# Kernel tuning notes

Measured on AMD Instinct MI355X. Metric: run time of the kernel, lower is better.

Reference implementation:

```python
import jax, jax.numpy as jnp
import numpy as np

K = 20  # top-K neighbors per stock
SLOPE = 0.2  # LeakyReLU negative slope


def _gru_layer(x, Wih, Whh, bih, bhh):
    # x: [N, T, D]; PyTorch GRU gate order: r, z, n
    H = Whh.shape[1]
    def step(h, xt):
        gi = xt @ Wih.T + bih            # [N, 3H]
        gh = h @ Whh.T + bhh             # [N, 3H]
        ir, iz, inn = jnp.split(gi, 3, axis=1)
        hr, hz, hn = jnp.split(gh, 3, axis=1)
        r = jax.nn.sigmoid(ir + hr)
        z = jax.nn.sigmoid(iz + hz)
        n = jnp.tanh(inn + r * hn)
        h_new = (1.0 - z) * n + z * h
        return h_new, h_new
    h0 = jnp.zeros((x.shape[0], H), x.dtype)
    _, ys = jax.lax.scan(step, h0, jnp.swapaxes(x, 0, 1))
    return jnp.swapaxes(ys, 0, 1)        # [N, T, H]


def _cos_sim(x, y):
    # torch: xy / (||x|| ||y||^T), NaN (0/0) replaced by 0
    xy = x @ y.T
    xn = jnp.sqrt(jnp.sum(x * x, axis=1, keepdims=True))
    yn = jnp.sqrt(jnp.sum(y * y, axis=1, keepdims=True))
    denom = xn @ yn.T
    safe = jnp.where(denom == 0.0, 1.0, denom)
    return jnp.where(denom == 0.0, 0.0, xy / safe)


def setup_inputs() -> dict:
    key = jax.random.key(0)
    ks = jax.random.split(key, 20)
    N, T, F, H = 4096, 64, 32, 128
    def rn(k, shape, scale=0.1):
        return jax.random.normal(k, shape, dtype=jnp.float32) * scale
    b01 = lambda n: jnp.full((n,), 0.1, jnp.float32)
    return {
        'x': jax.random.normal(ks[0], (N, T, F), dtype=jnp.float32),
        'Wih0': rn(ks[1], (3 * H, F)), 'Whh0': rn(ks[2], (3 * H, H)),
        'bih0': rn(ks[3], (3 * H,)), 'bhh0': rn(ks[4], (3 * H,)),
        'Wih1': rn(ks[5], (3 * H, H)), 'Whh1': rn(ks[6], (3 * H, H)),
        'bih1': rn(ks[7], (3 * H,)), 'bhh1': rn(ks[8], (3 * H,)),
        'W_hc': rn(ks[9], (H, H)), 'b_hc': b01(H),
        'W_hs': rn(ks[10], (H, H)), 'b_hs': b01(H),
        'W_fore': rn(ks[11], (H, H)), 'b_fore': b01(H),
        'W_back': rn(ks[12], (H, H)), 'b_back': b01(H),
        'W_indi': rn(ks[13], (H, H)), 'b_indi': b01(H),
        'W_out': rn(ks[14], (1, H)), 'b_out': b01(1),
    }


def reference(x, Wih0, Whh0, bih0, bhh0, Wih1, Whh1, bih1, bhh1,
              W_hc, b_hc, W_hs, b_hs, W_fore, b_fore, W_back, b_back,
              W_indi, b_indi, W_out, b_out):
    lrelu = lambda v: jax.nn.leaky_relu(v, SLOPE)
    h = _gru_layer(x, Wih0, Whh0, bih0, bhh0)
    h = _gru_layer(h, Wih1, Whh1, bih1, bhh1)
    g = h[:, -1, :]                                   # [N, H] last-step GRU output
    N = g.shape[0]

    sim = _cos_sim(g, g)                              # [N, N]
    diag = jnp.diagonal(sim)
    sim_off = sim * (1.0 - jnp.eye(N, dtype=sim.dtype))

    # top-K (by |sim|) neighbor mask via scatter
    cols = jax.lax.top_k(jnp.abs(sim_off), K)[1]      # [N, K]
    rows = jnp.repeat(jnp.arange(N), K)
    mask = jnp.zeros((N, N), sim.dtype).at[rows, cols.reshape(-1)].set(1.0)

    tks = sim_off * mask
    col_nz = (jnp.sum(tks, axis=0) != 0).astype(sim.dtype)
    tks = tks + jnp.diag(col_nz * diag)

    # concept features; zero rows (empty concepts) are masked instead of filtered
    concept_raw = tks.T @ g                           # [N, H]
    valid = (jnp.sum(concept_raw, axis=1) != 0).astype(g.dtype)
    cf = lrelu(concept_raw @ W_hc.T + b_hc) * valid[:, None]

    attn = jax.nn.softmax(_cos_sim(g, cf), axis=0)    # softmax over stocks per concept
    hs = lrelu((attn @ cf) @ W_hs.T + b_hs)
    back = lrelu(hs @ W_back.T + b_back)
    fore = lrelu(hs @ W_fore.T + b_fore)
    indi = lrelu((g - back) @ W_indi.T + b_indi)
    pred = (fore + indi) @ W_out.T + b_out            # [N, 1]
    return pred.squeeze(-1)
```

## Files before the change

### kernel.cpp

```cpp
#include <hip/hip_runtime.h>


typedef float f32x4 __attribute__((ext_vector_type(4)));
typedef short s16x8 __attribute__((ext_vector_type(8)));
typedef unsigned short u16;
typedef unsigned long long u64;

#define DEVFN static __device__ __forceinline__

DEVFN u16 f2bf(float f) {
  union { float f; unsigned u; } v; v.f = f;
  return (u16)((v.u + 0x7FFFu + ((v.u >> 16) & 1u)) >> 16);
}

DEVFN f32x4 mfma16(s16x8 a, s16x8 b, f32x4 c) {
  return __builtin_amdgcn_mfma_f32_16x16x32_bf16(a, b, c, 0, 0, 0);
}

DEVFN float sigmf(float x) { return __builtin_amdgcn_rcpf(1.f + __expf(-x)); }
DEVFN float tanhf_fast(float x) {
  float e = __expf(2.f * x);
  return 1.f - 2.f * __builtin_amdgcn_rcpf(e + 1.f);
}
DEVFN float lrelu(float v) { return v > 0.f ? v : 0.2f * v; }

__global__ void cvt_all(const float* __restrict__ w0, const float* __restrict__ w1,
                        const float* __restrict__ w2, const float* __restrict__ w3,
                        const float* __restrict__ w4, const float* __restrict__ w5,
                        const float* __restrict__ w6, const float* __restrict__ w7,
                        u16* __restrict__ dst) {
  int i = blockIdx.x * 256 + threadIdx.x;
  if (i >= 225280) return;
  float v;
  if      (i < 12288)  v = w0[i];
  else if (i < 61440)  v = w1[i - 12288];
  else if (i < 110592) v = w2[i - 61440];
  else if (i < 159744) v = w3[i - 110592];
  else if (i < 176128) v = w4[i - 159744];
  else if (i < 192512) v = w5[i - 176128];
  else if (i < 208896) v = w6[i - 192512];
  else                 v = w7[i - 208896];
  dst[i] = f2bf(v);
}

__launch_bounds__(512, 2)
__global__ void gru_fused(const float* __restrict__ x,
                          const u16* __restrict__ Wih0, const u16* __restrict__ Whh0,
                          const float* __restrict__ bih0, const float* __restrict__ bhh0,
                          const u16* __restrict__ Wih1, const u16* __restrict__ Whh1,
                          const float* __restrict__ bih1, const float* __restrict__ bhh1,
                          float* __restrict__ g_out)
{
  const int tid  = threadIdx.x;
  const int w    = tid >> 6;
  const int l    = tid & 63;
  const int quad = l >> 4;
  const int l16  = l & 15;
  const int r0   = blockIdx.x * 16;
  const int c    = w * 16 + l16;

  __shared__ u16 sh_x[16 * 40];
  __shared__ u16 sh_h0[2][16 * 136];
  __shared__ u16 sh_h1[2][16 * 136];

  s16x8 B0ih[3];
  s16x8 B0hh[3][4];
  s16x8 B1ih[3][4];
  s16x8 B1hh[3][4];
  float bi0[3], bh0[3], bi1[3], bh1[3];
#pragma unroll
  for (int g = 0; g < 3; ++g) {
    int j = g * 128 + c;
    bi0[g] = bih0[j]; bh0[g] = bhh0[j];
    bi1[g] = bih1[j]; bh1[g] = bhh1[j];
    B0ih[g] = *(const s16x8*)(Wih0 + j * 32 + quad * 8);
#pragma unroll
    for (int kk = 0; kk < 4; ++kk) {
      B0hh[g][kk] = *(const s16x8*)(Whh0 + j * 128 + kk * 32 + quad * 8);
      B1ih[g][kk] = *(const s16x8*)(Wih1 + j * 128 + kk * 32 + quad * 8);
      B1hh[g][kk] = *(const s16x8*)(Whh1 + j * 128 + kk * 32 + quad * 8);
    }
  }
  float h0reg[4] = {0.f, 0.f, 0.f, 0.f};
  float h1reg[4] = {0.f, 0.f, 0.f, 0.f};
  for (int idx = tid; idx < 16 * 136; idx += 512) {
    sh_h0[0][idx] = 0; sh_h1[0][idx] = 0;
  }
  const int xr = tid >> 5, xc = tid & 31;
  float xpre = x[(size_t)(r0 + xr) * 2048 + xc];
  __syncthreads();

  const f32x4 zz4 = {0.f, 0.f, 0.f, 0.f};
  for (int t = 0; t < 64; ++t) {
    const int cur = t & 1, nxt = cur ^ 1;
    sh_x[xr * 40 + xc] = f2bf(xpre);
    __syncthreads();
    s16x8 ax = *(const s16x8*)(sh_x + l16 * 40 + quad * 8);
    s16x8 ah0[4], ah1[4];
#pragma unroll
    for (int kk = 0; kk < 4; ++kk) {
      ah0[kk] = *(const s16x8*)(sh_h0[cur] + l16 * 136 + kk * 32 + quad * 8);
      ah1[kk] = *(const s16x8*)(sh_h1[cur] + l16 * 136 + kk * 32 + quad * 8);
    }
    if (t < 63) xpre = x[(size_t)(r0 + xr) * 2048 + (t + 1) * 32 + xc];

    {
      f32x4 ai[3], ah[3];
#pragma unroll
      for (int g = 0; g < 3; ++g) { ai[g] = mfma16(ax, B0ih[g], zz4); ah[g] = zz4; }
#pragma unroll
      for (int g = 0; g < 3; ++g)
#pragma unroll
        for (int kk = 0; kk < 4; ++kk) ah[g] = mfma16(ah0[kk], B0hh[g][kk], ah[g]);
#pragma unroll
      for (int i = 0; i < 4; ++i) {
        int m = quad * 4 + i;
        float rr = sigmf(ai[0][i] + bi0[0] + ah[0][i] + bh0[0]);
        float zg = sigmf(ai[1][i] + bi0[1] + ah[1][i] + bh0[1]);
        float nn = tanhf_fast(ai[2][i] + bi0[2] + rr * (ah[2][i] + bh0[2]));
        float hnew = (1.f - zg) * nn + zg * h0reg[i];
        h0reg[i] = hnew;
        sh_h0[nxt][m * 136 + c] = f2bf(hnew);
      }
    }
    __syncthreads();
    {
      s16x8 a1x[4];
#pragma unroll
      for (int kk = 0; kk < 4; ++kk)
        a1x[kk] = *(const s16x8*)(sh_h0[nxt] + l16 * 136 + kk * 32 + quad * 8);
      f32x4 ai[3], ah[3];
#pragma unroll
      for (int g = 0; g < 3; ++g) { ai[g] = zz4; ah[g] = zz4; }
#pragma unroll
      for (int g = 0; g < 3; ++g)
#pragma unroll
        for (int kk = 0; kk < 4; ++kk) {
          ai[g] = mfma16(a1x[kk], B1ih[g][kk], ai[g]);
          ah[g] = mfma16(ah1[kk], B1hh[g][kk], ah[g]);
        }
#pragma unroll
      for (int i = 0; i < 4; ++i) {
        int m = quad * 4 + i;
        float rr = sigmf(ai[0][i] + bi1[0] + ah[0][i] + bh1[0]);
        float zg = sigmf(ai[1][i] + bi1[1] + ah[1][i] + bh1[1]);
        float nn = tanhf_fast(ai[2][i] + bi1[2] + rr * (ah[2][i] + bh1[2]));
        float hnew = (1.f - zg) * nn + zg * h1reg[i];
        h1reg[i] = hnew;
        sh_h1[nxt][m * 136 + c] = f2bf(hnew);
        if (t == 63) g_out[(size_t)(r0 + m) * 128 + c] = hnew;
      }
    }
  }
}

__global__ void norm_cvt(const float* __restrict__ src, u16* __restrict__ dst,
                         float* __restrict__ rn)
{
  const int tid = threadIdx.x;
  const int wv = tid >> 6, l = tid & 63;
  const int row = blockIdx.x * 4 + wv;
  float2 f2 = *(const float2*)(src + (size_t)row * 128 + l * 2);
  float s = f2.x * f2.x + f2.y * f2.y;
#pragma unroll
  for (int off = 32; off >= 1; off >>= 1) s += __shfl_xor(s, off);
  ushort2 p; p.x = f2bf(f2.x); p.y = f2bf(f2.y);
  *(ushort2*)(dst + (size_t)row * 128 + l * 2) = p;
  if (l == 0) rn[row] = (s == 0.f) ? 0.f : rsqrtf(s);
}

template<int MODE>
__launch_bounds__(256, 1)
__global__ void cos_gemm(const u16* __restrict__ A, const u16* __restrict__ B,
                         const float* __restrict__ rnA, const float* __restrict__ rnB,
                         float* __restrict__ C, u16* __restrict__ E,
                         float* __restrict__ colsum)
{
  __shared__ u16 shA[128 * 136];
  __shared__ u16 shB[128 * 136];
  const int tid = threadIdx.x;
  const int l = tid & 63, wv = tid >> 6;
  const int quad = l >> 4, l16 = l & 15;
  const int i0 = blockIdx.y * 128, j0 = blockIdx.x * 128;
  {
    int r = tid >> 1, half = tid & 1;
    const int4* sa = (const int4*)(A + (size_t)(i0 + r) * 128 + half * 64);
    int4* da = (int4*)(shA + r * 136 + half * 64);
    const int4* sb = (const int4*)(B + (size_t)(j0 + r) * 128 + half * 64);
    int4* db = (int4*)(shB + r * 136 + half * 64);
#pragma unroll
    for (int q = 0; q < 8; ++q) { da[q] = sa[q]; db[q] = sb[q]; }
  }
  __syncthreads();
  const int wm = wv >> 1, wn = wv & 1;
  f32x4 acc[4][4];
  const f32x4 zz4 = {0.f, 0.f, 0.f, 0.f};
#pragma unroll
  for (int a = 0; a < 4; ++a)
#pragma unroll
    for (int b = 0; b < 4; ++b) acc[a][b] = zz4;
#pragma unroll
  for (int kk = 0; kk < 4; ++kk) {
    s16x8 af[4], bfr[4];
#pragma unroll
    for (int mt = 0; mt < 4; ++mt)
      af[mt] = *(const s16x8*)(shA + (wm * 64 + mt * 16 + l16) * 136 + kk * 32 + quad * 8);
#pragma unroll
    for (int nt = 0; nt < 4; ++nt)
      bfr[nt] = *(const s16x8*)(shB + (wn * 64 + nt * 16 + l16) * 136 + kk * 32 + quad * 8);
#pragma unroll
    for (int mt = 0; mt < 4; ++mt)
#pragma unroll
      for (int nt = 0; nt < 4; ++nt) acc[mt][nt] = mfma16(af[mt], bfr[nt], acc[mt][nt]);
  }
  float ra[4][4];
#pragma unroll
  for (int mt = 0; mt < 4; ++mt)
#pragma unroll
    for (int i = 0; i < 4; ++i) ra[mt][i] = rnA[i0 + wm * 64 + mt * 16 + quad * 4 + i];
#pragma unroll
  for (int nt = 0; nt < 4; ++nt) {
    int col = j0 + wn * 64 + nt * 16 + l16;
    float rb = rnB[col];
    float psum = 0.f;
#pragma unroll
    for (int mt = 0; mt < 4; ++mt)
#pragma unroll
      for (int i = 0; i < 4; ++i) {
        int row = i0 + wm * 64 + mt * 16 + quad * 4 + i;
        float v = acc[mt][nt][i] * ra[mt][i] * rb;
        if constexpr (MODE == 0) {
          C[(size_t)row * 4096 + col] = v;
        } else {
          float e = __expf(v);
          E[(size_t)row * 4096 + col] = f2bf(e);
          psum += e;
        }
      }
    if constexpr (MODE == 1) {
      psum += __shfl_xor(psum, 16);
      psum += __shfl_xor(psum, 32);
      if (quad == 0) atomicAdd(colsum + col, psum);
    }
  }
}

__launch_bounds__(256, 1)
__global__ void topk_select(const float* __restrict__ sim,
                            int* __restrict__ gselj, float* __restrict__ gselv,
                            int* __restrict__ cnt, int* __restrict__ touched)
{
  __shared__ unsigned hist[2048];
  __shared__ u64 cand[3072];
  __shared__ int selj[20];
  __shared__ unsigned ws4[4];
  __shared__ int shb, shcnt;
  const int tid = threadIdx.x;
  const int row = blockIdx.x;
  const int l = tid & 63, wv = tid >> 6;

  for (int i = tid; i < 2048; i += 256) hist[i] = 0;
  if (tid == 0) shcnt = 0;
  __syncthreads();

  unsigned key[4][4];
#pragma unroll
  for (int q = 0; q < 4; ++q) {
    int e0 = (q * 256 + tid) * 4;
    float4 v = *(const float4*)(sim + (size_t)row * 4096 + e0);
    key[q][0] = (e0 + 0 == row) ? 0u : (__float_as_uint(v.x) & 0x7FFFFFFFu);
    key[q][1] = (e0 + 1 == row) ? 0u : (__float_as_uint(v.y) & 0x7FFFFFFFu);
    key[q][2] = (e0 + 2 == row) ? 0u : (__float_as_uint(v.z) & 0x7FFFFFFFu);
    key[q][3] = (e0 + 3 == row) ? 0u : (__float_as_uint(v.w) & 0x7FFFFFFFu);
#pragma unroll
    for (int c = 0; c < 4; ++c) {
      unsigned bin = key[q][c] >> 19; if (bin > 2047u) bin = 2047u;
      atomicAdd(&hist[bin], 1u);
    }
  }
  __syncthreads();

  unsigned s = 0;
#pragma unroll
  for (int j = 0; j < 8; ++j) s += hist[tid * 8 + j];
  unsigned r = s;
#pragma unroll
  for (int off = 1; off < 64; off <<= 1) {
    unsigned o = __shfl_down(r, off);
    if (l + off < 64) r += o;
  }
  if (l == 0) ws4[wv] = r;
  __syncthreads();
  unsigned upper = 0;
  for (int q = wv + 1; q < 4; ++q) upper += ws4[q];
  unsigned excl = upper + (r - s);
  if (excl < 20u && excl + s >= 20u) {
    unsigned cum = excl;
    for (int j = 7; j >= 0; --j) {
      cum += hist[tid * 8 + j];
      if (cum >= 20u) { shb = tid * 8 + j; break; }
    }
  }
  __syncthreads();
  const unsigned b = (unsigned)shb;

#pragma unroll
  for (int q = 0; q < 4; ++q) {
    int e0 = (q * 256 + tid) * 4;
#pragma unroll
    for (int c = 0; c < 4; ++c) {
      unsigned bin = key[q][c] >> 19; if (bin > 2047u) bin = 2047u;
      if (bin >= b) {
        int p = atomicAdd(&shcnt, 1);
        if (p < 3072) cand[p] = ((u64)key[q][c] << 32) | (u64)(4095 - (e0 + c));
      }
    }
  }
  __syncthreads();
  const int C = (shcnt < 3072) ? shcnt : 3072;

  if (wv == 0) {
    for (int it = 0; it < 20; ++it) {
      u64 best = 0ull; int bpos = -1;
      for (int p = l; p < C; p += 64) {
        u64 cv = cand[p];
        if (cv > best) { best = cv; bpos = p; }
      }
      u64 mine = best;
#pragma unroll
      for (int off = 1; off < 64; off <<= 1) {
        u64 o = __shfl_xor(best, off);
        if (o > best) best = o;
      }
      if (mine == best && bpos >= 0 && best != 0ull) cand[bpos] = 0ull;
      if (l == 0) selj[it] = 4095 - (int)(best & 0xFFFull);
    }
  }
  __syncthreads();
  if (tid < 20) {
    int idx = selj[tid];
    float sv = (idx == row) ? 0.f : sim[(size_t)row * 4096 + idx];
    gselj[row * 20 + tid] = idx;
    gselv[row * 20 + tid] = sv;
    atomicAdd(&cnt[idx], 1);
    if (sv != 0.f) atomicOr(touched + idx, 1);
  }
}

__launch_bounds__(1024, 1)
__global__ void scan4096(const int* __restrict__ cnt, int* __restrict__ offs,
                         int* __restrict__ cur)
{
  __shared__ int wsum[16];
  const int t = threadIdx.x, l = t & 63, wv = t >> 6;
  int4 c = ((const int4*)cnt)[t];
  int s = c.x + c.y + c.z + c.w;
  int ps = s;
#pragma unroll
  for (int off = 1; off < 64; off <<= 1) {
    int o = __shfl_up(ps, off);
    if (l >= off) ps += o;
  }
  if (l == 63) wsum[wv] = ps;
  __syncthreads();
  if (t == 0) {
    int a = 0;
#pragma unroll
    for (int q = 0; q < 16; ++q) { int x = wsum[q]; wsum[q] = a; a += x; }
  }
  __syncthreads();
  int base = wsum[wv] + (ps - s);
  int4 o4;
  o4.x = base; o4.y = o4.x + c.x; o4.z = o4.y + c.y; o4.w = o4.z + c.z;
  ((int4*)offs)[t] = o4;
  ((int4*)cur)[t] = o4;
}

__global__ void scatter_entries(const int* __restrict__ gselj, const float* __restrict__ gselv,
                                int* __restrict__ cur, int* __restrict__ eid,
                                float* __restrict__ ev)
{
  unsigned idx = blockIdx.x * 256 + threadIdx.x;
  unsigned row = idx / 20u;
  int j = gselj[idx]; float v = gselv[idx];
  int pos = atomicAdd(&cur[j], 1);
  eid[pos] = (int)row; ev[pos] = v;
}

__launch_bounds__(128, 1)
__global__ void concept_cf(const int* __restrict__ offs, const int* __restrict__ cnt,
                           const int* __restrict__ eid, const float* __restrict__ ev,
                           const float* __restrict__ g, const float* __restrict__ sim,
                           const int* __restrict__ touched,
                           const float* __restrict__ Whc, const float* __restrict__ bhc,
                           float* __restrict__ cf, u16* __restrict__ cfbf,
                           float* __restrict__ rncf)
{
  __shared__ float shc[128];
  __shared__ float red2[2];
  const int j = blockIdx.x, d = threadIdx.x;
  const int l = d & 63, wv = d >> 6;
  const int off = offs[j], n = cnt[j];
  float acc = 0.f;
  for (int p = 0; p < n; ++p) {
    int i = eid[off + p]; float v = ev[off + p];
    acc += v * g[(size_t)i * 128 + d];
  }
  if (touched[j]) acc += sim[(size_t)j * 4097] * g[(size_t)j * 128 + d];
  float s = acc;
#pragma unroll
  for (int o = 32; o >= 1; o >>= 1) s += __shfl_xor(s, o);
  if (l == 0) red2[wv] = s;
  shc[d] = acc;
  __syncthreads();
  float valid = ((red2[0] + red2[1]) != 0.f) ? 1.f : 0.f;
  float o = bhc[d];
  const float4* wr = (const float4*)(Whc + (size_t)d * 128);
#pragma unroll 8
  for (int q = 0; q < 32; ++q) {
    float4 w4 = wr[q];
    float4 c4 = *((const float4*)shc + q);
    o += c4.x * w4.x + c4.y * w4.y + c4.z * w4.z + c4.w * w4.w;
  }
  float cfv = lrelu(o) * valid;
  cf[(size_t)j * 128 + d] = cfv;
  cfbf[(size_t)j * 128 + d] = f2bf(cfv);
  __syncthreads();
  float nn = cfv * cfv;
#pragma unroll
  for (int of = 32; of >= 1; of >>= 1) nn += __shfl_xor(nn, of);
  if (l == 0) red2[wv] = nn;
  __syncthreads();
  if (d == 0) {
    float q2 = red2[0] + red2[1];
    rncf[j] = (q2 == 0.f) ? 0.f : rsqrtf(q2);
  }
}

__global__ void scale_cfT(const float* __restrict__ cf, const float* __restrict__ colsum,
                          u16* __restrict__ cfTs)
{
  int idx = blockIdx.x * 256 + threadIdx.x;
  int n = idx >> 12, c = idx & 4095;
  float rz = __builtin_amdgcn_rcpf(colsum[c]);
  cfTs[idx] = f2bf(cf[(size_t)c * 128 + n] * rz);
}

__launch_bounds__(256, 1)
__global__ void attn_cf(const u16* __restrict__ attn, const u16* __restrict__ cfT,
                        float* __restrict__ hs_pre)
{
  __shared__ u16 shw[16 * 136];
  const int tid = threadIdx.x;
  const int l = tid & 63, wv = tid >> 6;
  const int quad = l >> 4, l16 = l & 15;
  const int r0 = blockIdx.x * 16;
  f32x4 acc[2];
  const f32x4 zz4 = {0.f, 0.f, 0.f, 0.f};
  acc[0] = zz4; acc[1] = zz4;
  for (int kc = 0; kc < 32; ++kc) {
    if (kc) __syncthreads();
    {
      int r = tid >> 4, seg = tid & 15;
      *(int4*)(shw + r * 136 + seg * 8) =
        *(const int4*)(attn + (size_t)(r0 + r) * 4096 + kc * 128 + seg * 8);
    }
    __syncthreads();
#pragma unroll
    for (int kk = 0; kk < 4; ++kk) {
      s16x8 a = *(const s16x8*)(shw + l16 * 136 + kk * 32 + quad * 8);
#pragma unroll
      for (int nt = 0; nt < 2; ++nt) {
        int n = wv * 32 + nt * 16 + l16;
        s16x8 b = *(const s16x8*)(cfT + (size_t)n * 4096 + kc * 128 + kk * 32 + quad * 8);
        acc[nt] = mfma16(a, b, acc[nt]);
      }
    }
  }
#pragma unroll
  for (int nt = 0; nt < 2; ++nt)
#pragma unroll
    for (int i = 0; i < 4; ++i) {
      int row = r0 + quad * 4 + i;
      int col = wv * 32 + nt * 16 + l16;
      hs_pre[(size_t)row * 128 + col] = acc[nt][i];
    }
}

__launch_bounds__(256, 1)
__global__ void head_kernel(const float* __restrict__ hs_pre, const float* __restrict__ g,
                            const u16* __restrict__ whs, const u16* __restrict__ wfore,
                            const u16* __restrict__ wback, const u16* __restrict__ windi,
                            const float* __restrict__ b_hs, const float* __restrict__ b_fore,
                            const float* __restrict__ b_back, const float* __restrict__ b_indi,
                            const float* __restrict__ W_out, const float* __restrict__ b_out,
                            float* __restrict__ outp)
{
  __shared__ u16 bufin[16 * 136];
  __shared__ u16 bufB[16 * 136];
  __shared__ float bufF[16 * 132];
  __shared__ float shWout[128];
  const int tid = threadIdx.x;
  const int l = tid & 63, wv = tid >> 6;
  const int quad = l >> 4, l16 = l & 15;
  const int r0 = blockIdx.x * 16;
  const f32x4 zz4 = {0.f, 0.f, 0.f, 0.f};

  if (tid < 128) shWout[tid] = W_out[tid];
  for (int idx = tid; idx < 2048; idx += 256) {
    int j = idx >> 7, n = idx & 127;
    bufin[j * 136 + n] = f2bf(hs_pre[(size_t)(r0 + j) * 128 + n]);
  }
  __syncthreads();
  {
    s16x8 a[4];
#pragma unroll
    for (int kk = 0; kk < 4; ++kk)
      a[kk] = *(const s16x8*)(bufin + l16 * 136 + kk * 32 + quad * 8);
    f32x4 acc[2]; acc[0] = zz4; acc[1] = zz4;
#pragma unroll
    for (int nt = 0; nt < 2; ++nt) {
      int n = wv * 32 + nt * 16 + l16;
#pragma unroll
      for (int kk = 0; kk < 4; ++kk)
        acc[nt] = mfma16(a[kk], *(const s16x8*)(whs + n * 128 + kk * 32 + quad * 8), acc[nt]);
    }
#pragma unroll
    for (int nt = 0; nt < 2; ++nt) {
      int n = wv * 32 + nt * 16 + l16;
      float bb = b_hs[n];
#pragma unroll
      for (int i = 0; i < 4; ++i)
        bufB[(quad * 4 + i) * 136 + n] = f2bf(lrelu(acc[nt][i] + bb));
    }
  }
  __syncthreads();
  {
    s16x8 a[4];
#pragma unroll
    for (int kk = 0; kk < 4; ++kk)
      a[kk] = *(const s16x8*)(bufB + l16 * 136 + kk * 32 + quad * 8);
    f32x4 aF[2], aB[2]; aF[0] = zz4; aF[1] = zz4; aB[0] = zz4; aB[1] = zz4;
#pragma unroll
    for (int nt = 0; nt < 2; ++nt) {
      int n = wv * 32 + nt * 16 + l16;
#pragma unroll
      for (int kk = 0; kk < 4; ++kk) {
        aF[nt] = mfma16(a[kk], *(const s16x8*)(wfore + n * 128 + kk * 32 + quad * 8), aF[nt]);
        aB[nt] = mfma16(a[kk], *(const s16x8*)(wback + n * 128 + kk * 32 + quad * 8), aB[nt]);
      }
    }
#pragma unroll
    for (int nt = 0; nt < 2; ++nt) {
      int n = wv * 32 + nt * 16 + l16;
      float bf_ = b_fore[n], bb_ = b_back[n];
#pragma unroll
      for (int i = 0; i < 4; ++i) {
        int m = quad * 4 + i;
        bufF[m * 132 + n] = lrelu(aF[nt][i] + bf_);
        float back = lrelu(aB[nt][i] + bb_);
        float gv = g[(size_t)(r0 + m) * 128 + n];
        bufin[m * 136 + n] = f2bf(gv - back);
      }
    }
  }
  __syncthreads();
  {
    s16x8 a[4];
#pragma unroll
    for (int kk = 0; kk < 4; ++kk)
      a[kk] = *(const s16x8*)(bufin + l16 * 136 + kk * 32 + quad * 8);
    f32x4 acc[2]; acc[0] = zz4; acc[1] = zz4;
#pragma unroll
    for (int nt = 0; nt < 2; ++nt) {
      int n = wv * 32 + nt * 16 + l16;
#pragma unroll
      for (int kk = 0; kk < 4; ++kk)
        acc[nt] = mfma16(a[kk], *(const s16x8*)(windi + n * 128 + kk * 32 + quad * 8), acc[nt]);
    }
#pragma unroll
    for (int nt = 0; nt < 2; ++nt) {
      int n = wv * 32 + nt * 16 + l16;
      float bi_ = b_indi[n];
#pragma unroll
      for (int i = 0; i < 4; ++i)
        bufF[(quad * 4 + i) * 132 + n] += lrelu(acc[nt][i] + bi_);
    }
  }
  __syncthreads();
  if (tid < 16) {
    float s = b_out[0];
    const float* fr = bufF + tid * 132;
    for (int n = 0; n < 128; ++n) s += fr[n] * shWout[n];
    outp[r0 + tid] = s;
  }
}

static const size_t OFF_A       = 0;
static const size_t OFF_ATTN    = 67108864;
static const size_t OFF_G       = 100663296;
static const size_t OFF_GBF     = 102760448;
static const size_t OFF_RNG     = 103809024;
static const size_t OFF_SELJ    = 103825408;
static const size_t OFF_SELV    = 104153088;
static const size_t OFF_EID     = 104480768;
static const size_t OFF_EV      = 104808448;
static const size_t OFF_CNT     = 105136128;
static const size_t OFF_TOUCH   = 105152512;
static const size_t OFF_COLSUM  = 105168896;
static const size_t OFF_OFFS    = 105185280;
static const size_t OFF_CUR     = 105201664;
static const size_t OFF_CF      = 105218048;
static const size_t OFF_CFBF    = 107315200;
static const size_t OFF_CFTS    = 108363776;
static const size_t OFF_RNCF    = 109412352;
static const size_t OFF_HSPRE   = 109428736;
static const size_t OFF_WB      = 111525888;

extern "C" void kernel_launch(void* const* d_in, const int* in_sizes, int n_in,
                              void* d_out, int out_size, void* d_ws, size_t ws_size,
                              hipStream_t stream)
{
  (void)in_sizes; (void)n_in; (void)out_size; (void)ws_size;
  const float* x      = (const float*)d_in[0];
  const float* Wih0   = (const float*)d_in[1];
  const float* Whh0   = (const float*)d_in[2];
  const float* bih0   = (const float*)d_in[3];
  const float* bhh0   = (const float*)d_in[4];
  const float* Wih1   = (const float*)d_in[5];
  const float* Whh1   = (const float*)d_in[6];
  const float* bih1   = (const float*)d_in[7];
  const float* bhh1   = (const float*)d_in[8];
  const float* W_hc   = (const float*)d_in[9];
  const float* b_hc   = (const float*)d_in[10];
  const float* W_hs   = (const float*)d_in[11];
  const float* b_hs   = (const float*)d_in[12];
  const float* W_fore = (const float*)d_in[13];
  const float* b_fore = (const float*)d_in[14];
  const float* W_back = (const float*)d_in[15];
  const float* b_back = (const float*)d_in[16];
  const float* W_indi = (const float*)d_in[17];
  const float* b_indi = (const float*)d_in[18];
  const float* W_out  = (const float*)d_in[19];
  const float* b_out  = (const float*)d_in[20];

  char* ws = (char*)d_ws;
  float* simbuf  = (float*)(ws + OFF_A);
  u16*   attnb   = (u16*)(ws + OFF_ATTN);
  float* gbuf    = (float*)(ws + OFF_G);
  u16*   gbf     = (u16*)(ws + OFF_GBF);
  float* rng     = (float*)(ws + OFF_RNG);
  int*   gselj   = (int*)(ws + OFF_SELJ);
  float* gselv   = (float*)(ws + OFF_SELV);
  int*   eid     = (int*)(ws + OFF_EID);
  float* ev      = (float*)(ws + OFF_EV);
  int*   cntb    = (int*)(ws + OFF_CNT);
  int*   touched = (int*)(ws + OFF_TOUCH);
  float* colsum  = (float*)(ws + OFF_COLSUM);
  int*   offsb   = (int*)(ws + OFF_OFFS);
  int*   curb    = (int*)(ws + OFF_CUR);
  float* cf      = (float*)(ws + OFF_CF);
  u16*   cfbf    = (u16*)(ws + OFF_CFBF);
  u16*   cfTs    = (u16*)(ws + OFF_CFTS);
  float* rncf    = (float*)(ws + OFF_RNCF);
  float* hs_pre  = (float*)(ws + OFF_HSPRE);
  u16*   wsB     = (u16*)(ws + OFF_WB);
  u16 *wih0b = wsB, *whh0b = wsB + 12288, *wih1b = wsB + 61440, *whh1b = wsB + 110592;
  u16 *whsb = wsB + 159744, *wforeb = wsB + 176128, *wbackb = wsB + 192512, *windib = wsB + 208896;

  cvt_all<<<880, 256, 0, stream>>>(Wih0, Whh0, Wih1, Whh1, W_hs, W_fore, W_back, W_indi, wsB);

  gru_fused<<<256, 512, 0, stream>>>(x, wih0b, whh0b, bih0, bhh0,
                                     wih1b, whh1b, bih1, bhh1, gbuf);

  norm_cvt<<<1024, 256, 0, stream>>>(gbuf, gbf, rng);
  cos_gemm<0><<<dim3(32, 32), 256, 0, stream>>>(gbf, gbf, rng, rng, simbuf,
                                                (u16*)nullptr, (float*)nullptr);

  hipMemsetAsync(ws + OFF_CNT, 0, 49152, stream);
  topk_select<<<4096, 256, 0, stream>>>(simbuf, gselj, gselv, cntb, touched);
  scan4096<<<1, 1024, 0, stream>>>(cntb, offsb, curb);
  scatter_entries<<<320, 256, 0, stream>>>(gselj, gselv, curb, eid, ev);
  concept_cf<<<4096, 128, 0, stream>>>(offsb, cntb, eid, ev, gbuf, simbuf, touched,
                                       W_hc, b_hc, cf, cfbf, rncf);

  cos_gemm<1><<<dim3(32, 32), 256, 0, stream>>>(gbf, cfbf, rng, rncf, (float*)nullptr,
                                                attnb, colsum);
  scale_cfT<<<2048, 256, 0, stream>>>(cf, colsum, cfTs);
  attn_cf<<<256, 256, 0, stream>>>(attnb, cfTs, hs_pre);

  head_kernel<<<256, 256, 0, stream>>>(hs_pre, gbuf, whsb, wforeb, wbackb, windib,
                                       b_hs, b_fore, b_back, b_indi, W_out, b_out,
                                       (float*)d_out);
}
```

Before: 444.5 us.

## Skew GRU layers by one timestep to drop a barrier per step

Restructures the two-layer GRU recurrence as a wavefront: layer 1 at step t-1 and layer 0 at step t now run in the same iteration, both reading the previous shared-memory h buffers. This removes one __syncthreads per timestep and lets all MFMAs of both layers issue back to back. A prologue handles layer 0 at t=0 and an epilogue handles layer 1's last step. Input and hidden biases for the r and z gates are pre-summed, and the x staging buffer is double-buffered. The cost is more live accumulator registers per iteration, which could pressure occupancy under the 512x2 launch bounds.

New measurement: 447.6 us. No clear change (+0.7%).

```diff
diff --git a/kernel.cpp b/kernel.cpp
--- a/kernel.cpp
+++ b/kernel.cpp
@@ -59,7 +59,7 @@
   const int r0   = blockIdx.x * 16;
   const int c    = w * 16 + l16;
 
-  __shared__ u16 sh_x[16 * 40];
+  __shared__ u16 sh_x[2][16 * 40];
   __shared__ u16 sh_h0[2][16 * 136];
   __shared__ u16 sh_h1[2][16 * 136];
 
@@ -67,12 +67,17 @@
   s16x8 B0hh[3][4];
   s16x8 B1ih[3][4];
   s16x8 B1hh[3][4];
-  float bi0[3], bh0[3], bi1[3], bh1[3];
+  float brz0[2], bin0, bhn0, brz1[2], bin1, bhn1;
+  {
+    int j0g = c, j1g = 128 + c, j2g = 256 + c;
+    brz0[0] = bih0[j0g] + bhh0[j0g];  brz0[1] = bih0[j1g] + bhh0[j1g];
+    bin0 = bih0[j2g];  bhn0 = bhh0[j2g];
+    brz1[0] = bih1[j0g] + bhh1[j0g];  brz1[1] = bih1[j1g] + bhh1[j1g];
+    bin1 = bih1[j2g];  bhn1 = bhh1[j2g];
+  }
 #pragma unroll
   for (int g = 0; g < 3; ++g) {
     int j = g * 128 + c;
-    bi0[g] = bih0[j]; bh0[g] = bhh0[j];
-    bi1[g] = bih1[j]; bh1[g] = bhh1[j];
     B0ih[g] = *(const s16x8*)(Wih0 + j * 32 + quad * 8);
 #pragma unroll
     for (int kk = 0; kk < 4; ++kk) {
@@ -83,73 +88,109 @@
   }
   float h0reg[4] = {0.f, 0.f, 0.f, 0.f};
   float h1reg[4] = {0.f, 0.f, 0.f, 0.f};
-  for (int idx = tid; idx < 16 * 136; idx += 512) {
-    sh_h0[0][idx] = 0; sh_h1[0][idx] = 0;
-  }
+  for (int idx = tid; idx < 16 * 136; idx += 512) sh_h1[0][idx] = 0;
+
   const int xr = tid >> 5, xc = tid & 31;
-  float xpre = x[(size_t)(r0 + xr) * 2048 + xc];
+  const float* xrow = x + (size_t)(r0 + xr) * 2048 + xc;
+  float xpre = xrow[0];
+  sh_x[0][xr * 40 + xc] = f2bf(xpre);
+  xpre = xrow[32];
   __syncthreads();
 
   const f32x4 zz4 = {0.f, 0.f, 0.f, 0.f};
-  for (int t = 0; t < 64; ++t) {
+  {
+    s16x8 ax = *(const s16x8*)(sh_x[0] + l16 * 40 + quad * 8);
+    f32x4 ai[3];
+#pragma unroll
+    for (int g = 0; g < 3; ++g) ai[g] = mfma16(ax, B0ih[g], zz4);
+#pragma unroll
+    for (int i = 0; i < 4; ++i) {
+      int m = quad * 4 + i;
+      float rr = sigmf(ai[0][i] + brz0[0]);
+      float zg = sigmf(ai[1][i] + brz0[1]);
+      float nn = tanhf_fast(ai[2][i] + bin0 + rr * bhn0);
+      float hnew = nn - zg * nn;
+      h0reg[i] = hnew;
+      sh_h0[0][m * 136 + c] = f2bf(hnew);
+    }
+  }
+
+  for (int t = 0; t < 63; ++t) {
     const int cur = t & 1, nxt = cur ^ 1;
-    sh_x[xr * 40 + xc] = f2bf(xpre);
+    sh_x[nxt][xr * 40 + xc] = f2bf(xpre);
     __syncthreads();
-    s16x8 ax = *(const s16x8*)(sh_x + l16 * 40 + quad * 8);
+
     s16x8 ah0[4], ah1[4];
 #pragma unroll
     for (int kk = 0; kk < 4; ++kk) {
       ah0[kk] = *(const s16x8*)(sh_h0[cur] + l16 * 136 + kk * 32 + quad * 8);
       ah1[kk] = *(const s16x8*)(sh_h1[cur] + l16 * 136 + kk * 32 + quad * 8);
     }
-    if (t < 63) xpre = x[(size_t)(r0 + xr) * 2048 + (t + 1) * 32 + xc];
-
-    {
-      f32x4 ai[3], ah[3];
-#pragma unroll
-      for (int g = 0; g < 3; ++g) { ai[g] = mfma16(ax, B0ih[g], zz4); ah[g] = zz4; }
-#pragma unroll
-      for (int g = 0; g < 3; ++g)
-#pragma unroll
-        for (int kk = 0; kk < 4; ++kk) ah[g] = mfma16(ah0[kk], B0hh[g][kk], ah[g]);
-#pragma unroll
-      for (int i = 0; i < 4; ++i) {
-        int m = quad * 4 + i;
-        float rr = sigmf(ai[0][i] + bi0[0] + ah[0][i] + bh0[0]);
-        float zg = sigmf(ai[1][i] + bi0[1] + ah[1][i] + bh0[1]);
-        float nn = tanhf_fast(ai[2][i] + bi0[2] + rr * (ah[2][i] + bh0[2]));
-        float hnew = (1.f - zg) * nn + zg * h0reg[i];
-        h0reg[i] = hnew;
-        sh_h0[nxt][m * 136 + c] = f2bf(hnew);
-      }
-    }
-    __syncthreads();
-    {
-      s16x8 a1x[4];
-#pragma unroll
-      for (int kk = 0; kk < 4; ++kk)
-        a1x[kk] = *(const s16x8*)(sh_h0[nxt] + l16 * 136 + kk * 32 + quad * 8);
-      f32x4 ai[3], ah[3];
-#pragma unroll
-      for (int g = 0; g < 3; ++g) { ai[g] = zz4; ah[g] = zz4; }
-#pragma unroll
-      for (int g = 0; g < 3; ++g)
-#pragma unroll
-        for (int kk = 0; kk < 4; ++kk) {
-          ai[g] = mfma16(a1x[kk], B1ih[g][kk], ai[g]);
-          ah[g] = mfma16(ah1[kk], B1hh[g][kk], ah[g]);
-        }
-#pragma unroll
-      for (int i = 0; i < 4; ++i) {
-        int m = quad * 4 + i;
-        float rr = sigmf(ai[0][i] + bi1[0] + ah[0][i] + bh1[0]);
-        float zg = sigmf(ai[1][i] + bi1[1] + ah[1][i] + bh1[1]);
-        float nn = tanhf_fast(ai[2][i] + bi1[2] + rr * (ah[2][i] + bh1[2]));
-        float hnew = (1.f - zg) * nn + zg * h1reg[i];
-        h1reg[i] = hnew;
-        sh_h1[nxt][m * 136 + c] = f2bf(hnew);
-        if (t == 63) g_out[(size_t)(r0 + m) * 128 + c] = hnew;
-      }
+    s16x8 ax = *(const s16x8*)(sh_x[nxt] + l16 * 40 + quad * 8);
+    if (t <= 61) xpre = xrow[(t + 2) * 32];
+
+    f32x4 i1[3], a1[3], i0[3], a0[3];
+#pragma unroll
+    for (int g = 0; g < 3; ++g) { i1[g] = zz4; a1[g] = zz4; a0[g] = zz4; }
+#pragma unroll
+    for (int g = 0; g < 3; ++g) i0[g] = mfma16(ax, B0ih[g], zz4);
+#pragma unroll
+    for (int g = 0; g < 3; ++g)
+#pragma unroll
+      for (int kk = 0; kk < 4; ++kk) {
+        i1[g] = mfma16(ah0[kk], B1ih[g][kk], i1[g]);
+        a1[g] = mfma16(ah1[kk], B1hh[g][kk], a1[g]);
+        a0[g] = mfma16(ah0[kk], B0hh[g][kk], a0[g]);
+      }
+
+#pragma unroll
+    for (int i = 0; i < 4; ++i) {
+      int m = quad * 4 + i;
+      float rr = sigmf(i1[0][i] + a1[0][i] + brz1[0]);
+      float zg = sigmf(i1[1][i] + a1[1][i] + brz1[1]);
+      float nn = tanhf_fast(i1[2][i] + bin1 + rr * (a1[2][i] + bhn1));
+      float hnew = nn + zg * (h1reg[i] - nn);
+      h1reg[i] = hnew;
+      sh_h1[nxt][m * 136 + c] = f2bf(hnew);
+    }
+#pragma unroll
+    for (int i = 0; i < 4; ++i) {
+      int m = quad * 4 + i;
+      float rr = sigmf(i0[0][i] + a0[0][i] + brz0[0]);
+      float zg = sigmf(i0[1][i] + a0[1][i] + brz0[1]);
+      float nn = tanhf_fast(i0[2][i] + bin0 + rr * (a0[2][i] + bhn0));
+      float hnew = nn + zg * (h0reg[i] - nn);
+      h0reg[i] = hnew;
+      sh_h0[nxt][m * 136 + c] = f2bf(hnew);
+    }
+  }
+
+  __syncthreads();
+  {
+    s16x8 ah0[4], ah1[4];
+#pragma unroll
+    for (int kk = 0; kk < 4; ++kk) {
+      ah0[kk] = *(const s16x8*)(sh_h0[1] + l16 * 136 + kk * 32 + quad * 8);
+      ah1[kk] = *(const s16x8*)(sh_h1[1] + l16 * 136 + kk * 32 + quad * 8);
+    }
+    f32x4 i1[3], a1[3];
+#pragma unroll
+    for (int g = 0; g < 3; ++g) { i1[g] = zz4; a1[g] = zz4; }
+#pragma unroll
+    for (int g = 0; g < 3; ++g)
+#pragma unroll
+      for (int kk = 0; kk < 4; ++kk) {
+        i1[g] = mfma16(ah0[kk], B1ih[g][kk], i1[g]);
+        a1[g] = mfma16(ah1[kk], B1hh[g][kk], a1[g]);
+      }
+#pragma unroll
+    for (int i = 0; i < 4; ++i) {
+      int m = quad * 4 + i;
+      float rr = sigmf(i1[0][i] + a1[0][i] + brz1[0]);
+      float zg = sigmf(i1[1][i] + a1[1][i] + brz1[1]);
+      float nn = tanhf_fast(i1[2][i] + bin1 + rr * (a1[2][i] + bhn1));
+      float hnew = nn + zg * (h1reg[i] - nn);
+      g_out[(size_t)(r0 + m) * 128 + c] = hnew;
     }
   }
 }
```
